# Kernel tuning notes

Hardware: AMD Instinct MI355X
Metric: run time of the kernel (lower is better)

The kernel has to match this reference:

```python
import jax, jax.numpy as jnp
import numpy as np

D_IN, HID = 128, 256
N_A, N_T = 120000, 30000
E_AT, E_TA, E_AA = 2_000_000, 2_000_000, 3_000_000
OUTS = [("artist", 129), ("style", 32), ("genre", 18)]


def setup_inputs() -> dict:
    key = jax.random.key(0)
    ks = jax.random.split(key, 32)

    def w(k, shape, fan_in):
        return jax.random.normal(k, shape, jnp.float32) / np.float32(np.sqrt(fan_in))

    def edges(k, e, n_src, n_dst):
        k1, k2 = jax.random.split(k)
        return jnp.stack([jax.random.randint(k1, (e,), 0, n_src),
                          jax.random.randint(k2, (e,), 0, n_dst)]).astype(jnp.int32)

    inp = {}
    inp["x_artwork"] = jax.random.normal(ks[0], (N_A, D_IN), jnp.float32)
    inp["x_tag"] = jax.random.normal(ks[1], (N_T, D_IN), jnp.float32)
    inp["edge_at"] = edges(ks[2], E_AT, N_A, N_T)
    inp["edge_ta"] = edges(ks[3], E_TA, N_T, N_A)
    inp["edge_aa"] = edges(ks[4], E_AA, N_A, N_A)
    # layer-1 weights shared shape across 3 gnns (G) and 3 relations (R): [G,R,din,H]
    inp["Wl1"] = w(ks[5], (3, 3, D_IN, HID), D_IN)
    inp["Wr1"] = w(ks[6], (3, 3, D_IN, HID), D_IN)
    inp["b1"] = jnp.zeros((3, 3, HID), jnp.float32)
    for i, (name, o) in enumerate(OUTS):
        inp[f"Wl2_{name}"] = w(ks[7 + 3 * i], (3, HID, o), HID)
        inp[f"Wr2_{name}"] = w(ks[8 + 3 * i], (3, HID, o), HID)
        inp[f"b2_{name}"] = jnp.zeros((3, o), jnp.float32)
    return inp


def _seg_mean(feat, dst, n):
    # PyG mean aggregation: sum over in-edges / count, 0 for isolated nodes
    s = jax.ops.segment_sum(feat, dst, num_segments=n)
    c = jax.ops.segment_sum(jnp.ones((dst.shape[0], 1), feat.dtype), dst, num_segments=n)
    return s / jnp.maximum(c, 1.0)


def _hetero_sage(xa, xt, e_at, e_ta, e_aa, Wl, Wr, b):
    # Wl/Wr: [3, din, dout] (rel order: at, ta, aa), b: [3, dout]
    m_at = _seg_mean(xa[e_at[0]], e_at[1], xt.shape[0])
    h_t = m_at @ Wl[0] + b[0] + xt @ Wr[0]
    m_ta = _seg_mean(xt[e_ta[0]], e_ta[1], xa.shape[0])
    m_aa = _seg_mean(xa[e_aa[0]], e_aa[1], xa.shape[0])
    h_a = (m_ta @ Wl[1] + b[1] + xa @ Wr[1]) + (m_aa @ Wl[2] + b[2] + xa @ Wr[2])
    return h_a, h_t


def _dropout(x, key, rate=0.5):
    keep = jax.random.bernoulli(key, 1.0 - rate, x.shape)
    return jnp.where(keep, x / (1.0 - rate), jnp.zeros((), x.dtype))


def _gnn(g, xa, xt, e_at, e_ta, e_aa, Wl1, Wr1, b1, Wl2, Wr2, b2):
    h_a, h_t = _hetero_sage(xa, xt, e_at, e_ta, e_aa, Wl1, Wr1, b1)
    h_a, h_t = jax.nn.relu(h_a), jax.nn.relu(h_t)
    k1, k2 = jax.random.split(jax.random.fold_in(jax.random.key(42), g))
    h_a, h_t = _dropout(h_a, k1), _dropout(h_t, k2)
    o_a, o_t = _hetero_sage(h_a, h_t, e_at, e_ta, e_aa, Wl2, Wr2, b2)
    return jax.nn.log_softmax(o_a, axis=1), jax.nn.log_softmax(o_t, axis=1)


def reference(x_artwork, x_tag, edge_at, edge_ta, edge_aa, Wl1, Wr1, b1,
              Wl2_artist, Wr2_artist, b2_artist,
              Wl2_style, Wr2_style, b2_style,
              Wl2_genre, Wr2_genre, b2_genre):
    l2 = [(Wl2_artist, Wr2_artist, b2_artist),
          (Wl2_style, Wr2_style, b2_style),
          (Wl2_genre, Wr2_genre, b2_genre)]
    outs = []
    for g in range(3):
        Wl2, Wr2, b2 = l2[g]
        o_a, o_t = _gnn(g, x_artwork, x_tag, edge_at, edge_ta, edge_aa,
                        Wl1[g], Wr1[g], b1[g], Wl2, Wr2, b2)
        outs.extend([o_a, o_t])
    return tuple(outs)
```

## Files before the change

### kernel.cpp

```cpp
#include <hip/hip_runtime.h>
#include <stdint.h>
#include <stddef.h>

typedef unsigned short bf16;
typedef __attribute__((ext_vector_type(8))) short short8;
typedef __attribute__((ext_vector_type(4))) float f32x4;

__device__ __forceinline__ float bf2f(unsigned short u){
  union { uint32_t i; float f; } x; x.i = ((uint32_t)u) << 16; return x.f;
}
__device__ __forceinline__ unsigned short f2bf(float f){
  union { float f; uint32_t i; } x; x.f = f;
  uint32_t r = x.i + 0x7FFFu + ((x.i >> 16) & 1u);
  return (unsigned short)(r >> 16);
}
__device__ __forceinline__ uint32_t pk2(float a, float b){
  return (uint32_t)f2bf(a) | ((uint32_t)f2bf(b) << 16);
}

__device__ __forceinline__ uint8_t f2fp8(float f){
  uint32_t b = __float_as_uint(f);
  uint32_t s = (b >> 24) & 0x80u;
  uint32_t x = b & 0x7fffffffu;
  if (x >= 0x43e00000u) return (uint8_t)(s | 0x7eu);
  if (x < 0x3c800000u){
    uint32_t q = (uint32_t)rintf(__uint_as_float(x) * 512.f);
    return (uint8_t)(s | q);
  }
  uint32_t lsb = (x >> 20) & 1u;
  x += 0x7ffffu + lsb;
  uint32_t u = (((x >> 23) - 120u) << 3) | ((x >> 20) & 7u);
  if (u > 0x7eu) u = 0x7eu;
  return (uint8_t)(s | u);
}
__device__ __forceinline__ float fp8d(uint8_t u){
  uint32_t e = (u >> 3) & 15u, m = u & 7u;
  float v = (e == 0) ? (float)m * 0.001953125f
                     : ldexpf((float)(8u + m), (int)e - 10);
  return (u & 0x80u) ? -v : v;
}

__host__ __device__ __forceinline__ uint32_t rotl32_(uint32_t x, int d){
  return (x << d) | (x >> (32 - d));
}
__host__ __device__ inline void tf2x32(uint32_t k0, uint32_t k1, uint32_t x0, uint32_t x1,
                                       uint32_t* o0, uint32_t* o1){
  uint32_t k2 = k0 ^ k1 ^ 0x1BD11BDAu;
#define TF_R4(ra,rb,rc,rd) \
  x0 += x1; x1 = rotl32_(x1,ra); x1 ^= x0; \
  x0 += x1; x1 = rotl32_(x1,rb); x1 ^= x0; \
  x0 += x1; x1 = rotl32_(x1,rc); x1 ^= x0; \
  x0 += x1; x1 = rotl32_(x1,rd); x1 ^= x0;
  x0 += k0; x1 += k1;
  TF_R4(13,15,26,6)  x0 += k1; x1 += k2 + 1u;
  TF_R4(17,29,16,24) x0 += k2; x1 += k0 + 2u;
  TF_R4(13,15,26,6)  x0 += k0; x1 += k1 + 3u;
  TF_R4(17,29,16,24) x0 += k1; x1 += k2 + 4u;
  TF_R4(13,15,26,6)  x0 += k2; x1 += k0 + 5u;
  *o0 = x0; *o1 = x1;
#undef TF_R4
}

__global__ void k_zeroi(int* __restrict__ p, int n){
  int i = blockIdx.x * 256 + threadIdx.x;
  if (i < n) p[i] = 0;
}
__global__ void k_f2bf(const float* __restrict__ in, bf16* __restrict__ out, int n4){
  int i = blockIdx.x * 256 + threadIdx.x;
  if (i < n4){
    float4 v = ((const float4*)in)[i];
    ushort4 u; u.x = f2bf(v.x); u.y = f2bf(v.y); u.z = f2bf(v.z); u.w = f2bf(v.w);
    ((ushort4*)out)[i] = u;
  }
}

__global__ void k_deg(const int* __restrict__ dst, int* __restrict__ deg, int E){
  int i = blockIdx.x * 256 + threadIdx.x;
  if (i < E) atomicAdd(&deg[dst[i]], 1);
}
__global__ __launch_bounds__(256)
void k_scan_partial(const int* __restrict__ in, int* __restrict__ exc,
                    int* __restrict__ bsum, int n){
  __shared__ int tmp[256];
  int t = threadIdx.x, i = blockIdx.x * 256 + t;
  int v = (i < n) ? in[i] : 0;
  tmp[t] = v; __syncthreads();
  #pragma unroll
  for (int off = 1; off < 256; off <<= 1){
    int u = (t >= off) ? tmp[t - off] : 0; __syncthreads();
    tmp[t] += u; __syncthreads();
  }
  if (i < n) exc[i] = tmp[t] - v;
  if (t == 255) bsum[blockIdx.x] = tmp[255];
}
__global__ __launch_bounds__(1024)
void k_scan_bsum(int* __restrict__ bsum, int nb, int* __restrict__ total_out){
  __shared__ int tmp[1024];
  int t = threadIdx.x;
  int v = (t < nb) ? bsum[t] : 0;
  tmp[t] = v; __syncthreads();
  #pragma unroll
  for (int off = 1; off < 1024; off <<= 1){
    int u = (t >= off) ? tmp[t - off] : 0; __syncthreads();
    tmp[t] += u; __syncthreads();
  }
  if (t < nb) bsum[t] = tmp[t] - v;
  if (t == 1023) *total_out = tmp[1023];
}
__global__ void k_scan_add(int* __restrict__ exc, const int* __restrict__ bsum, int n){
  int i = blockIdx.x * 256 + threadIdx.x;
  if (i < n) exc[i] += bsum[blockIdx.x];
}
__global__ void k_fill(const int* __restrict__ src, const int* __restrict__ dst,
                       const int* __restrict__ rs, int* __restrict__ cur,
                       int* __restrict__ cs, int E){
  int i = blockIdx.x * 256 + threadIdx.x;
  if (i < E){
    int d = dst[i];
    int p = atomicAdd(&cur[d], 1);
    cs[rs[d] + p] = src[i];
  }
}

__global__ __launch_bounds__(64)
void k_agg128b(const bf16* __restrict__ X, const int* __restrict__ rs,
               const int* __restrict__ cs, bf16* __restrict__ out){
  int node = blockIdx.x, lane = threadIdx.x;
  int s0 = rs[node], s1 = rs[node + 1];
  float ax = 0.f, ay = 0.f;
  int e = s0;
  for (; e + 4 <= s1; e += 4){
    int c0 = cs[e], c1 = cs[e+1], c2 = cs[e+2], c3 = cs[e+3];
    uint32_t v0 = ((const uint32_t*)(X + (size_t)c0 * 128))[lane];
    uint32_t v1 = ((const uint32_t*)(X + (size_t)c1 * 128))[lane];
    uint32_t v2 = ((const uint32_t*)(X + (size_t)c2 * 128))[lane];
    uint32_t v3 = ((const uint32_t*)(X + (size_t)c3 * 128))[lane];
    ax += bf2f((unsigned short)(v0 & 0xffffu)) + bf2f((unsigned short)(v1 & 0xffffu))
        + bf2f((unsigned short)(v2 & 0xffffu)) + bf2f((unsigned short)(v3 & 0xffffu));
    ay += bf2f((unsigned short)(v0 >> 16)) + bf2f((unsigned short)(v1 >> 16))
        + bf2f((unsigned short)(v2 >> 16)) + bf2f((unsigned short)(v3 >> 16));
  }
  for (; e < s1; ++e){
    uint32_t v = ((const uint32_t*)(X + (size_t)cs[e] * 128))[lane];
    ax += bf2f((unsigned short)(v & 0xffffu));
    ay += bf2f((unsigned short)(v >> 16));
  }
  float inv = 1.f / fmaxf((float)(s1 - s0), 1.f);
  ((uint32_t*)(out + (size_t)node * 128))[lane] = pk2(ax * inv, ay * inv);
}

__global__ void k_wt1a(const float* __restrict__ Wl1g, const float* __restrict__ Wr1g,
                       bf16* __restrict__ dst){
  int n = blockIdx.y, k = blockIdx.x * 128 + threadIdx.x;
  int seg = k >> 7, kk = k & 127;
  float v;
  if (seg == 0)      v = Wl1g[(size_t)(128 + kk) * 256 + n];
  else if (seg == 1) v = Wl1g[(size_t)(256 + kk) * 256 + n];
  else               v = Wr1g[(size_t)(128 + kk) * 256 + n] + Wr1g[(size_t)(256 + kk) * 256 + n];
  dst[(size_t)n * 384 + k] = f2bf(v);
}
__global__ void k_wt1t(const float* __restrict__ Wl1g, const float* __restrict__ Wr1g,
                       bf16* __restrict__ dst){
  int n = blockIdx.y, k = blockIdx.x * 128 + threadIdx.x;
  int kk = k & 127;
  float v = (k < 128) ? Wl1g[(size_t)kk * 256 + n] : Wr1g[(size_t)kk * 256 + n];
  dst[(size_t)n * 256 + k] = f2bf(v);
}
__global__ void k_wt2a(const float* __restrict__ Wl2g, const float* __restrict__ Wr2g,
                       int O, bf16* __restrict__ dst){
  int n = blockIdx.y, k = blockIdx.x * 128 + threadIdx.x;
  int strip = n / O, r = n - strip * O;
  float v;
  if (strip == 0)      v = Wl2g[(size_t)k * O + r];
  else if (strip == 1) v = Wl2g[(size_t)512 * O + (size_t)k * O + r];
  else                 v = Wr2g[(size_t)256 * O + (size_t)k * O + r]
                         + Wr2g[(size_t)512 * O + (size_t)k * O + r];
  dst[(size_t)n * 256 + k] = f2bf(v);
}
__global__ void k_wt2t(const float* __restrict__ Wl2g, const float* __restrict__ Wr2g,
                       int O, bf16* __restrict__ dst){
  int n = blockIdx.y, k = blockIdx.x * 128 + threadIdx.x;
  int strip = n / O, r = n - strip * O;
  float v = (strip == 0) ? Wl2g[(size_t)256 * O + (size_t)k * O + r]
                         : Wr2g[(size_t)k * O + r];
  dst[(size_t)n * 256 + k] = f2bf(v);
}
__global__ void k_bias(const float* __restrict__ b1g, const float* __restrict__ b2g,
                       int O, float* __restrict__ bc1, float* __restrict__ bc2){
  int t = threadIdx.x;
  bc1[t] = b1g[256 + t] + b1g[512 + t];
  if (t < O) bc2[t] = b2g[O + t] + b2g[2 * O + t];
}

template<int EPI>
__global__ __launch_bounds__(256)
void k_gemm_mfma(const bf16* __restrict__ A0, const bf16* __restrict__ A1,
                 const bf16* __restrict__ A2, int lda,
                 const bf16* __restrict__ Bt, int ldb,
                 int M, int N, int Ktot,
                 bf16* __restrict__ hC,
                 uint8_t* __restrict__ z0, uint8_t* __restrict__ z1,
                 float* __restrict__ outF, const float* __restrict__ bias,
                 int O, int zoff, uint32_t dk0, uint32_t dk1){
  __shared__ bf16 As[128][40];
  __shared__ bf16 Bs[64][40];
  const int tid = threadIdx.x;
  const int w = tid >> 6, l = tid & 63;
  const int r0 = blockIdx.y * 128, c0 = blockIdx.x * 64;

  f32x4 acc[2][4] = {};

  const int sm = tid >> 1, sk = (tid & 1) * 16;
  const int bn = tid >> 2, bk = (tid & 3) * 8;
  const int arow = r0 + sm, brow = c0 + bn;
  const int lr = l & 15, g8 = (l >> 4) * 8;

  for (int kk = 0; kk < Ktot; kk += 32){
    const int seg = kk >> 7, koff = (kk & 127) + sk;
    const bf16* Ap = (seg == 0) ? A0 : ((seg == 1) ? A1 : A2);
    uint4 wa0 = {0,0,0,0}, wa1 = {0,0,0,0};
    if (arow < M){
      const uint4* p = (const uint4*)(Ap + (size_t)arow * lda + koff);
      wa0 = p[0]; wa1 = p[1];
    }
    uint4 wb = {0,0,0,0};
    if (brow < N) wb = *(const uint4*)(Bt + (size_t)brow * ldb + kk + bk);
    __syncthreads();
    *(uint4*)&As[sm][sk]     = wa0;
    *(uint4*)&As[sm][sk + 8] = wa1;
    *(uint4*)&Bs[bn][bk]     = wb;
    __syncthreads();
    short8 a0 = *(const short8*)&As[w * 32      + lr][g8];
    short8 a1 = *(const short8*)&As[w * 32 + 16 + lr][g8];
    short8 b0 = *(const short8*)&Bs[     lr][g8];
    short8 b1 = *(const short8*)&Bs[16 + lr][g8];
    short8 b2 = *(const short8*)&Bs[32 + lr][g8];
    short8 b3 = *(const short8*)&Bs[48 + lr][g8];
    acc[0][0] = __builtin_amdgcn_mfma_f32_16x16x32_bf16(a0, b0, acc[0][0], 0, 0, 0);
    acc[0][1] = __builtin_amdgcn_mfma_f32_16x16x32_bf16(a0, b1, acc[0][1], 0, 0, 0);
    acc[0][2] = __builtin_amdgcn_mfma_f32_16x16x32_bf16(a0, b2, acc[0][2], 0, 0, 0);
    acc[0][3] = __builtin_amdgcn_mfma_f32_16x16x32_bf16(a0, b3, acc[0][3], 0, 0, 0);
    acc[1][0] = __builtin_amdgcn_mfma_f32_16x16x32_bf16(a1, b0, acc[1][0], 0, 0, 0);
    acc[1][1] = __builtin_amdgcn_mfma_f32_16x16x32_bf16(a1, b1, acc[1][1], 0, 0, 0);
    acc[1][2] = __builtin_amdgcn_mfma_f32_16x16x32_bf16(a1, b2, acc[1][2], 0, 0, 0);
    acc[1][3] = __builtin_amdgcn_mfma_f32_16x16x32_bf16(a1, b3, acc[1][3], 0, 0, 0);
  }
  #pragma unroll
  for (int rt = 0; rt < 2; ++rt){
    #pragma unroll
    for (int ct = 0; ct < 4; ++ct){
      #pragma unroll
      for (int r = 0; r < 4; ++r){
        int row = r0 + w * 32 + rt * 16 + (l >> 4) * 4 + r;
        int col = c0 + ct * 16 + lr;
        if (row < M && col < N){
          float v = acc[rt][ct][r];
          if (EPI == 0){
            v += bias[col];
            uint32_t o0, o1;
            tf2x32(dk0, dk1, 0u, (uint32_t)(row * 256 + col), &o0, &o1);
            float a = fmaxf(v, 0.f) * 2.f;
            hC[(size_t)row * 256 + col] = ((o0 ^ o1) >> 31) ? (bf16)0 : f2bf(a);
          } else {
            int s = (col >= O) + (EPI == 1 ? (col >= 2 * O) : 0);
            int lc = col - s * O;
            const int fs = (EPI == 1) ? 2 : 1;
            if (s == fs){
              outF[(size_t)row * O + lc] = v + bias[lc];
            } else {
              uint8_t* d = (s == 0) ? z0 : z1;
              d[(size_t)row * 192 + zoff + lc] = f2fp8(v);
            }
          }
        }
      }
    }
  }
}

__global__ __launch_bounds__(192)
void k_assemble_t(const uint8_t* __restrict__ z, const int* __restrict__ rs,
                  const int* __restrict__ cs,
                  float* __restrict__ o0, float* __restrict__ o1, float* __restrict__ o2){
  __shared__ float lut[256];
  __shared__ float sb[179];
  __shared__ float lse[3];
  const int node = blockIdx.x, t = threadIdx.x;
  lut[t] = fp8d((uint8_t)t);
  if (t < 64) lut[t + 192] = fp8d((uint8_t)(t + 192));
  const bool act = t < 179;
  const int h = (t < 129) ? 0 : ((t < 161) ? 1 : 2);
  const int base = (h == 0) ? 0 : ((h == 1) ? 129 : 161);
  const int Oh = (h == 0) ? 129 : ((h == 1) ? 32 : 18);
  const int s0 = rs[node], s1 = rs[node + 1];
  __syncthreads();
  float acc = 0.f;
  int e = s0;
  for (; e + 4 <= s1; e += 4){
    size_t c0 = (size_t)cs[e] * 192, c1 = (size_t)cs[e+1] * 192;
    size_t c2 = (size_t)cs[e+2] * 192, c3 = (size_t)cs[e+3] * 192;
    if (act){
      float v0 = lut[z[c0 + t]], v1 = lut[z[c1 + t]];
      float v2 = lut[z[c2 + t]], v3 = lut[z[c3 + t]];
      acc += (v0 + v1) + (v2 + v3);
    }
  }
  for (; e < s1; ++e)
    if (act) acc += lut[z[(size_t)cs[e] * 192 + t]];
  const float inv = 1.f / fmaxf((float)(s1 - s0), 1.f);
  float* orow = ((h == 0) ? o0 : ((h == 1) ? o1 : o2)) + (size_t)node * Oh + (t - base);
  float v = 0.f;
  if (act) v = *orow + acc * inv;
  if (act) sb[t] = v;
  __syncthreads();
  const int wv = t >> 6, ln = t & 63;
  {
    const int b = (wv == 0) ? 0 : ((wv == 1) ? 129 : 161);
    const int W = (wv == 0) ? 129 : ((wv == 1) ? 32 : 18);
    float m = -3.4e38f;
    for (int i = ln; i < W; i += 64) m = fmaxf(m, sb[b + i]);
    #pragma unroll
    for (int o = 32; o; o >>= 1) m = fmaxf(m, __shfl_xor(m, o));
    float s = 0.f;
    for (int i = ln; i < W; i += 64) s += expf(sb[b + i] - m);
    #pragma unroll
    for (int o = 32; o; o >>= 1) s += __shfl_xor(s, o);
    if (ln == 0) lse[wv] = m + logf(s);
  }
  __syncthreads();
  if (act) *orow = v - lse[h];
}

__global__ __launch_bounds__(192)
void k_assemble_a(const uint8_t* __restrict__ zT, const uint8_t* __restrict__ zA,
                  const int* __restrict__ rs_ta, const int* __restrict__ cs_ta,
                  const int* __restrict__ rs_aa, const int* __restrict__ cs_aa,
                  float* __restrict__ o0, float* __restrict__ o1, float* __restrict__ o2){
  __shared__ float lut[256];
  __shared__ float sb[179];
  __shared__ float lse[3];
  const int node = blockIdx.x, t = threadIdx.x;
  lut[t] = fp8d((uint8_t)t);
  if (t < 64) lut[t + 192] = fp8d((uint8_t)(t + 192));
  const bool act = t < 179;
  const int h = (t < 129) ? 0 : ((t < 161) ? 1 : 2);
  const int base = (h == 0) ? 0 : ((h == 1) ? 129 : 161);
  const int Oh = (h == 0) ? 129 : ((h == 1) ? 32 : 18);
  __syncthreads();
  float accT = 0.f, accA = 0.f;
  int s0 = rs_ta[node], s1 = rs_ta[node + 1];
  int e = s0;
  for (; e + 4 <= s1; e += 4){
    size_t c0 = (size_t)cs_ta[e] * 192, c1 = (size_t)cs_ta[e+1] * 192;
    size_t c2 = (size_t)cs_ta[e+2] * 192, c3 = (size_t)cs_ta[e+3] * 192;
    if (act){
      float v0 = lut[zT[c0 + t]], v1 = lut[zT[c1 + t]];
      float v2 = lut[zT[c2 + t]], v3 = lut[zT[c3 + t]];
      accT += (v0 + v1) + (v2 + v3);
    }
  }
  for (; e < s1; ++e)
    if (act) accT += lut[zT[(size_t)cs_ta[e] * 192 + t]];
  const float invT = 1.f / fmaxf((float)(s1 - s0), 1.f);
  s0 = rs_aa[node]; s1 = rs_aa[node + 1];
  e = s0;
  for (; e + 4 <= s1; e += 4){
    size_t c0 = (size_t)cs_aa[e] * 192, c1 = (size_t)cs_aa[e+1] * 192;
    size_t c2 = (size_t)cs_aa[e+2] * 192, c3 = (size_t)cs_aa[e+3] * 192;
    if (act){
      float v0 = lut[zA[c0 + t]], v1 = lut[zA[c1 + t]];
      float v2 = lut[zA[c2 + t]], v3 = lut[zA[c3 + t]];
      accA += (v0 + v1) + (v2 + v3);
    }
  }
  for (; e < s1; ++e)
    if (act) accA += lut[zA[(size_t)cs_aa[e] * 192 + t]];
  const float invA = 1.f / fmaxf((float)(s1 - s0), 1.f);
  float* orow = ((h == 0) ? o0 : ((h == 1) ? o1 : o2)) + (size_t)node * Oh + (t - base);
  float v = 0.f;
  if (act) v = *orow + accT * invT + accA * invA;
  if (act) sb[t] = v;
  __syncthreads();
  const int wv = t >> 6, ln = t & 63;
  {
    const int b = (wv == 0) ? 0 : ((wv == 1) ? 129 : 161);
    const int W = (wv == 0) ? 129 : ((wv == 1) ? 32 : 18);
    float m = -3.4e38f;
    for (int i = ln; i < W; i += 64) m = fmaxf(m, sb[b + i]);
    #pragma unroll
    for (int o = 32; o; o >>= 1) m = fmaxf(m, __shfl_xor(m, o));
    float s = 0.f;
    for (int i = ln; i < W; i += 64) s += expf(sb[b + i] - m);
    #pragma unroll
    for (int o = 32; o; o >>= 1) s += __shfl_xor(s, o);
    if (ln == 0) lse[wv] = m + logf(s);
  }
  __syncthreads();
  if (act) *orow = v - lse[h];
}

extern "C" void kernel_launch(void* const* d_in, const int* in_sizes, int n_in,
                              void* d_out, int out_size, void* d_ws, size_t ws_size,
                              hipStream_t stream){
  (void)n_in; (void)out_size; (void)ws_size;
  const float* xa  = (const float*)d_in[0];
  const float* xt  = (const float*)d_in[1];
  const int*   e_at = (const int*)d_in[2];
  const int*   e_ta = (const int*)d_in[3];
  const int*   e_aa = (const int*)d_in[4];
  const float* Wl1 = (const float*)d_in[5];
  const float* Wr1 = (const float*)d_in[6];
  const float* b1  = (const float*)d_in[7];
  const float* Wl2_[3] = {(const float*)d_in[8],  (const float*)d_in[11], (const float*)d_in[14]};
  const float* Wr2_[3] = {(const float*)d_in[9],  (const float*)d_in[12], (const float*)d_in[15]};
  const float* b2_[3]  = {(const float*)d_in[10], (const float*)d_in[13], (const float*)d_in[16]};

  const int NA = in_sizes[0] / 128;
  const int NT = in_sizes[1] / 128;
  const int EAT = in_sizes[2] / 2, ETA = in_sizes[3] / 2, EAA = in_sizes[4] / 2;
  const int Ov[3] = {129, 32, 18};
  const int og[3] = {0, 129, 161};

  char* Wp = (char*)d_ws;
  size_t off = 0;
  auto alloc = [&](size_t bytes)->char*{
    char* p = Wp + off; off = (off + bytes + 255) & ~(size_t)255; return p;
  };
  bf16* xa_b = (bf16*)alloc((size_t)NA * 128 * 2);
  bf16* xt_b = (bf16*)alloc((size_t)NT * 128 * 2);
  bf16* m_at = (bf16*)alloc((size_t)NT * 128 * 2);
  bf16* m_ta = (bf16*)alloc((size_t)NA * 128 * 2);
  bf16* m_aa = (bf16*)alloc((size_t)NA * 128 * 2);
  bf16* h_a  = (bf16*)alloc((size_t)NA * 256 * 2);
  bf16* h_t  = (bf16*)alloc((size_t)NT * 256 * 2);
  uint8_t* zA_at = (uint8_t*)alloc((size_t)NA * 192);
  uint8_t* zT_ta = (uint8_t*)alloc((size_t)NT * 192);
  uint8_t* zA_aa = (uint8_t*)alloc((size_t)NA * 192);
  bf16* Bt_ha = (bf16*)alloc((size_t)256 * 384 * 2);
  bf16* Bt_ht = (bf16*)alloc((size_t)256 * 256 * 2);
  bf16* BT2a  = (bf16*)alloc((size_t)3 * 129 * 256 * 2);
  bf16* BT2t  = (bf16*)alloc((size_t)2 * 129 * 256 * 2);
  float* bc1  = (float*)alloc(256 * 4);
  float* bc2  = (float*)alloc(129 * 4);
  int* rs_at  = (int*)alloc((size_t)(NT + 1) * 4);
  int* rs_ta  = (int*)alloc((size_t)(NA + 1) * 4);
  int* rs_aa  = (int*)alloc((size_t)(NA + 1) * 4);
  int* cur_at = (int*)alloc((size_t)NT * 4);
  int* cur_ta = (int*)alloc((size_t)NA * 4);
  int* cur_aa = (int*)alloc((size_t)NA * 4);
  int* bsum   = (int*)alloc(2048 * 4);
  int* cs_at  = (int*)alloc((size_t)EAT * 4);
  int* cs_ta  = (int*)alloc((size_t)ETA * 4);
  int* cs_aa  = (int*)alloc((size_t)EAA * 4);

  k_f2bf<<<(NA * 128 / 4 + 255) / 256, 256, 0, stream>>>(xa, xa_b, NA * 128 / 4);
  k_f2bf<<<(NT * 128 / 4 + 255) / 256, 256, 0, stream>>>(xt, xt_b, NT * 128 / 4);

  auto build_csr = [&](const int* edges, int E, int n, int* rs, int* cur, int* cs){
    int ebl = (E + 255) / 256, nbl = (n + 255) / 256;
    k_zeroi<<<nbl, 256, 0, stream>>>(cur, n);
    k_deg<<<ebl, 256, 0, stream>>>(edges + E, cur, E);
    k_scan_partial<<<nbl, 256, 0, stream>>>(cur, rs, bsum, n);
    k_scan_bsum<<<1, 1024, 0, stream>>>(bsum, nbl, rs + n);
    k_scan_add<<<nbl, 256, 0, stream>>>(rs, bsum, n);
    k_zeroi<<<nbl, 256, 0, stream>>>(cur, n);
    k_fill<<<ebl, 256, 0, stream>>>(edges, edges + E, rs, cur, cs, E);
  };
  build_csr(e_at, EAT, NT, rs_at, cur_at, cs_at);
  build_csr(e_ta, ETA, NA, rs_ta, cur_ta, cs_ta);
  build_csr(e_aa, EAA, NA, rs_aa, cur_aa, cs_aa);

  k_agg128b<<<NT, 64, 0, stream>>>(xa_b, rs_at, cs_at, m_at);
  k_agg128b<<<NA, 64, 0, stream>>>(xt_b, rs_ta, cs_ta, m_ta);
  k_agg128b<<<NA, 64, 0, stream>>>(xa_b, rs_aa, cs_aa, m_aa);

  size_t offA[3], offT[3], cum = 0;
  for (int g = 0; g < 3; ++g){
    offA[g] = cum; offT[g] = cum + (size_t)NA * Ov[g];
    cum += (size_t)(NA + NT) * Ov[g];
  }

  for (int g = 0; g < 3; ++g){
    const int O = Ov[g];
    float* outA = (float*)d_out + offA[g];
    float* outT = (float*)d_out + offT[g];
    const float* Wl1g = Wl1 + (size_t)(3 * g) * 128 * 256;
    const float* Wr1g = Wr1 + (size_t)(3 * g) * 128 * 256;
    const float* b1g  = b1  + (size_t)(3 * g) * 256;

    k_wt1a<<<dim3(3, 256), 128, 0, stream>>>(Wl1g, Wr1g, Bt_ha);
    k_wt1t<<<dim3(2, 256), 128, 0, stream>>>(Wl1g, Wr1g, Bt_ht);
    k_wt2a<<<dim3(2, 3 * O), 128, 0, stream>>>(Wl2_[g], Wr2_[g], O, BT2a);
    k_wt2t<<<dim3(2, 2 * O), 128, 0, stream>>>(Wl2_[g], Wr2_[g], O, BT2t);
    k_bias<<<1, 256, 0, stream>>>(b1g, b2_[g], O, bc1, bc2);

    uint32_t kg0, kg1, ka0, ka1, kt0, kt1;
    tf2x32(0u, 42u, 0u, (uint32_t)g, &kg0, &kg1);
    tf2x32(kg0, kg1, 0u, 0u, &ka0, &ka1);
    tf2x32(kg0, kg1, 0u, 1u, &kt0, &kt1);

    k_gemm_mfma<0><<<dim3(4, (NA + 127) / 128), 256, 0, stream>>>(
        m_ta, m_aa, xa_b, 128, Bt_ha, 384, NA, 256, 384,
        h_a, nullptr, nullptr, nullptr, bc1, 0, 0, ka0, ka1);
    k_gemm_mfma<0><<<dim3(4, (NT + 127) / 128), 256, 0, stream>>>(
        m_at, xt_b, xt_b, 128, Bt_ht, 256, NT, 256, 256,
        h_t, nullptr, nullptr, nullptr, b1g, 0, 0, kt0, kt1);

    k_gemm_mfma<1><<<dim3((3 * O + 63) / 64, (NA + 127) / 128), 256, 0, stream>>>(
        h_a, h_a + 128, h_a, 256, BT2a, 256, NA, 3 * O, 256,
        nullptr, zA_at, zA_aa, outA, bc2, O, og[g], 0, 0);
    k_gemm_mfma<2><<<dim3((2 * O + 63) / 64, (NT + 127) / 128), 256, 0, stream>>>(
        h_t, h_t + 128, h_t, 256, BT2t, 256, NT, 2 * O, 256,
        nullptr, zT_ta, nullptr, outT, b2_[g], O, og[g], 0, 0);
  }

  k_assemble_t<<<NT, 192, 0, stream>>>(zA_at, rs_at, cs_at,
                                       (float*)d_out + offT[0], (float*)d_out + offT[1],
                                       (float*)d_out + offT[2]);
  k_assemble_a<<<NA, 192, 0, stream>>>(zT_ta, zA_aa, rs_ta, cs_ta, rs_aa, cs_aa,
                                       (float*)d_out + offA[0], (float*)d_out + offA[1],
                                       (float*)d_out + offA[2]);
}
```

Baseline: 2.168 ms.

## Aggregate layer-1 neighbors from fp8 features, use hardware fp8 converts, widen GEMM tiles

```diff
diff --git a/kernel.cpp b/kernel.cpp
--- a/kernel.cpp
+++ b/kernel.cpp
@@ -18,7 +18,7 @@
   return (uint32_t)f2bf(a) | ((uint32_t)f2bf(b) << 16);
 }
 
-__device__ __forceinline__ uint8_t f2fp8(float f){
+__device__ __forceinline__ uint8_t f2fp8_sw(float f){
   uint32_t b = __float_as_uint(f);
   uint32_t s = (b >> 24) & 0x80u;
   uint32_t x = b & 0x7fffffffu;
@@ -33,11 +33,49 @@
   if (u > 0x7eu) u = 0x7eu;
   return (uint8_t)(s | u);
 }
+__device__ __forceinline__ float fp8_dec1_sw(uint32_t u){
+  uint32_t e = (u >> 3) & 15u, m = u & 7u;
+  float v = e ? __uint_as_float(((e + 120u) << 23) | (m << 20))
+              : (float)m * 0.001953125f;
+  return (u & 0x80u) ? -v : v;
+}
 __device__ __forceinline__ float fp8d(uint8_t u){
-  uint32_t e = (u >> 3) & 15u, m = u & 7u;
-  float v = (e == 0) ? (float)m * 0.001953125f
-                     : ldexpf((float)(8u + m), (int)e - 10);
-  return (u & 0x80u) ? -v : v;
+  return fp8_dec1_sw((uint32_t)u);
+}
+
+#if __has_builtin(__builtin_amdgcn_cvt_pk_f32_fp8) && __has_builtin(__builtin_amdgcn_cvt_pk_fp8_f32)
+#define FP8_HW 1
+#else
+#define FP8_HW 0
+#endif
+
+__device__ __forceinline__ void fp8_dec4(uint32_t w, float* o){
+#if FP8_HW
+  auto lo = __builtin_amdgcn_cvt_pk_f32_fp8((int)w, false);
+  auto hi = __builtin_amdgcn_cvt_pk_f32_fp8((int)w, true);
+  o[0] = lo[0]; o[1] = lo[1]; o[2] = hi[0]; o[3] = hi[1];
+#else
+  o[0] = fp8_dec1_sw(w & 0xffu);        o[1] = fp8_dec1_sw((w >> 8) & 0xffu);
+  o[2] = fp8_dec1_sw((w >> 16) & 0xffu); o[3] = fp8_dec1_sw(w >> 24);
+#endif
+}
+__device__ __forceinline__ uint8_t fp8_enc1(float v){
+#if FP8_HW
+  return (uint8_t)(__builtin_amdgcn_cvt_pk_fp8_f32(v, v, 0, false) & 0xff);
+#else
+  return f2fp8_sw(v);
+#endif
+}
+__device__ __forceinline__ uint32_t fp8_enc4(float a, float b, float c, float d){
+#if FP8_HW
+  int w = 0;
+  w = __builtin_amdgcn_cvt_pk_fp8_f32(a, b, w, false);
+  w = __builtin_amdgcn_cvt_pk_fp8_f32(c, d, w, true);
+  return (uint32_t)w;
+#else
+  return (uint32_t)f2fp8_sw(a) | ((uint32_t)f2fp8_sw(b) << 8)
+       | ((uint32_t)f2fp8_sw(c) << 16) | ((uint32_t)f2fp8_sw(d) << 24);
+#endif
 }
 
 __host__ __device__ __forceinline__ uint32_t rotl32_(uint32_t x, int d){
@@ -73,6 +111,13 @@
     ((ushort4*)out)[i] = u;
   }
 }
+__global__ void k_f2fp8(const float* __restrict__ in, uint8_t* __restrict__ out, int n4){
+  int i = blockIdx.x * 256 + threadIdx.x;
+  if (i < n4){
+    float4 v = ((const float4*)in)[i];
+    ((uint32_t*)out)[i] = fp8_enc4(v.x, v.y, v.z, v.w);
+  }
+}
 
 __global__ void k_deg(const int* __restrict__ dst, int* __restrict__ deg, int E){
   int i = blockIdx.x * 256 + threadIdx.x;
@@ -123,30 +168,38 @@
 }
 
 __global__ __launch_bounds__(64)
-void k_agg128b(const bf16* __restrict__ X, const int* __restrict__ rs,
-               const int* __restrict__ cs, bf16* __restrict__ out){
-  int node = blockIdx.x, lane = threadIdx.x;
-  int s0 = rs[node], s1 = rs[node + 1];
-  float ax = 0.f, ay = 0.f;
-  int e = s0;
-  for (; e + 4 <= s1; e += 4){
-    int c0 = cs[e], c1 = cs[e+1], c2 = cs[e+2], c3 = cs[e+3];
-    uint32_t v0 = ((const uint32_t*)(X + (size_t)c0 * 128))[lane];
-    uint32_t v1 = ((const uint32_t*)(X + (size_t)c1 * 128))[lane];
-    uint32_t v2 = ((const uint32_t*)(X + (size_t)c2 * 128))[lane];
-    uint32_t v3 = ((const uint32_t*)(X + (size_t)c3 * 128))[lane];
-    ax += bf2f((unsigned short)(v0 & 0xffffu)) + bf2f((unsigned short)(v1 & 0xffffu))
-        + bf2f((unsigned short)(v2 & 0xffffu)) + bf2f((unsigned short)(v3 & 0xffffu));
-    ay += bf2f((unsigned short)(v0 >> 16)) + bf2f((unsigned short)(v1 >> 16))
-        + bf2f((unsigned short)(v2 >> 16)) + bf2f((unsigned short)(v3 >> 16));
-  }
-  for (; e < s1; ++e){
-    uint32_t v = ((const uint32_t*)(X + (size_t)cs[e] * 128))[lane];
-    ax += bf2f((unsigned short)(v & 0xffffu));
-    ay += bf2f((unsigned short)(v >> 16));
-  }
-  float inv = 1.f / fmaxf((float)(s1 - s0), 1.f);
-  ((uint32_t*)(out + (size_t)node * 128))[lane] = pk2(ax * inv, ay * inv);
+void k_agg128_8(const uint8_t* __restrict__ X8, const int* __restrict__ rs,
+                const int* __restrict__ cs, bf16* __restrict__ out){
+  const int node = blockIdx.x, lane = threadIdx.x;
+  const int hl = lane >> 5, cl = lane & 31;
+  const int s0 = rs[node], s1 = rs[node + 1];
+  const int last = s1 - 1;
+  float a[4] = {0.f, 0.f, 0.f, 0.f};
+  for (int e = s0; e < s1; e += 8){
+    uint32_t w[4];
+    #pragma unroll
+    for (int j = 0; j < 4; ++j){
+      int i = e + j * 2 + hl;
+      int idx = (i < s1) ? i : last;
+      uint32_t ww = *(const uint32_t*)(X8 + (size_t)cs[idx] * 128 + (cl << 2));
+      w[j] = (i < s1) ? ww : 0u;
+    }
+    #pragma unroll
+    for (int j = 0; j < 4; ++j){
+      float d[4];
+      fp8_dec4(w[j], d);
+      a[0] += d[0]; a[1] += d[1]; a[2] += d[2]; a[3] += d[3];
+    }
+  }
+  #pragma unroll
+  for (int j = 0; j < 4; ++j) a[j] += __shfl_xor(a[j], 32);
+  if (lane < 32){
+    float inv = 1.f / fmaxf((float)(s1 - s0), 1.f);
+    ushort4 u;
+    u.x = f2bf(a[0] * inv); u.y = f2bf(a[1] * inv);
+    u.z = f2bf(a[2] * inv); u.w = f2bf(a[3] * inv);
+    *(ushort4*)(out + (size_t)node * 128 + (cl << 2)) = u;
+  }
 }
 
 __global__ void k_wt1a(const float* __restrict__ Wl1g, const float* __restrict__ Wr1g,
@@ -203,16 +256,16 @@
                  float* __restrict__ outF, const float* __restrict__ bias,
                  int O, int zoff, uint32_t dk0, uint32_t dk1){
   __shared__ bf16 As[128][40];
-  __shared__ bf16 Bs[64][40];
+  __shared__ bf16 Bs[128][40];
   const int tid = threadIdx.x;
   const int w = tid >> 6, l = tid & 63;
-  const int r0 = blockIdx.y * 128, c0 = blockIdx.x * 64;
-
-  f32x4 acc[2][4] = {};
+  const int wr = w >> 1, wc = w & 1;
+  const int r0 = blockIdx.y * 128, c0 = blockIdx.x * 128;
+
+  f32x4 acc[4][4] = {};
 
   const int sm = tid >> 1, sk = (tid & 1) * 16;
-  const int bn = tid >> 2, bk = (tid & 3) * 8;
-  const int arow = r0 + sm, brow = c0 + bn;
+  const int arow = r0 + sm, brow = c0 + sm;
   const int lr = l & 15, g8 = (l >> 4) * 8;
 
   for (int kk = 0; kk < Ktot; kk += 32){
@@ -223,36 +276,37 @@
       const uint4* p = (const uint4*)(Ap + (size_t)arow * lda + koff);
       wa0 = p[0]; wa1 = p[1];
     }
-    uint4 wb = {0,0,0,0};
-    if (brow < N) wb = *(const uint4*)(Bt + (size_t)brow * ldb + kk + bk);
+    uint4 wb0 = {0,0,0,0}, wb1 = {0,0,0,0};
+    if (brow < N){
+      const uint4* p = (const uint4*)(Bt + (size_t)brow * ldb + kk + sk);
+      wb0 = p[0]; wb1 = p[1];
+    }
     __syncthreads();
     *(uint4*)&As[sm][sk]     = wa0;
     *(uint4*)&As[sm][sk + 8] = wa1;
-    *(uint4*)&Bs[bn][bk]     = wb;
+    *(uint4*)&Bs[sm][sk]     = wb0;
+    *(uint4*)&Bs[sm][sk + 8] = wb1;
     __syncthreads();
-    short8 a0 = *(const short8*)&As[w * 32      + lr][g8];
-    short8 a1 = *(const short8*)&As[w * 32 + 16 + lr][g8];
-    short8 b0 = *(const short8*)&Bs[     lr][g8];
-    short8 b1 = *(const short8*)&Bs[16 + lr][g8];
-    short8 b2 = *(const short8*)&Bs[32 + lr][g8];
-    short8 b3 = *(const short8*)&Bs[48 + lr][g8];
-    acc[0][0] = __builtin_amdgcn_mfma_f32_16x16x32_bf16(a0, b0, acc[0][0], 0, 0, 0);
-    acc[0][1] = __builtin_amdgcn_mfma_f32_16x16x32_bf16(a0, b1, acc[0][1], 0, 0, 0);
-    acc[0][2] = __builtin_amdgcn_mfma_f32_16x16x32_bf16(a0, b2, acc[0][2], 0, 0, 0);
-    acc[0][3] = __builtin_amdgcn_mfma_f32_16x16x32_bf16(a0, b3, acc[0][3], 0, 0, 0);
-    acc[1][0] = __builtin_amdgcn_mfma_f32_16x16x32_bf16(a1, b0, acc[1][0], 0, 0, 0);
-    acc[1][1] = __builtin_amdgcn_mfma_f32_16x16x32_bf16(a1, b1, acc[1][1], 0, 0, 0);
-    acc[1][2] = __builtin_amdgcn_mfma_f32_16x16x32_bf16(a1, b2, acc[1][2], 0, 0, 0);
-    acc[1][3] = __builtin_amdgcn_mfma_f32_16x16x32_bf16(a1, b3, acc[1][3], 0, 0, 0);
+    short8 af[4], bf[4];
+    #pragma unroll
+    for (int f = 0; f < 4; ++f){
+      af[f] = *(const short8*)&As[wr * 64 + f * 16 + lr][g8];
+      bf[f] = *(const short8*)&Bs[wc * 64 + f * 16 + lr][g8];
+    }
+    #pragma unroll
+    for (int i = 0; i < 4; ++i)
+      #pragma unroll
+      for (int j = 0; j < 4; ++j)
+        acc[i][j] = __builtin_amdgcn_mfma_f32_16x16x32_bf16(af[i], bf[j], acc[i][j], 0, 0, 0);
   }
   #pragma unroll
-  for (int rt = 0; rt < 2; ++rt){
+  for (int rt = 0; rt < 4; ++rt){
     #pragma unroll
     for (int ct = 0; ct < 4; ++ct){
       #pragma unroll
       for (int r = 0; r < 4; ++r){
-        int row = r0 + w * 32 + rt * 16 + (l >> 4) * 4 + r;
-        int col = c0 + ct * 16 + lr;
+        int row = r0 + wr * 64 + rt * 16 + (l >> 4) * 4 + r;
+        int col = c0 + wc * 64 + ct * 16 + lr;
         if (row < M && col < N){
           float v = acc[rt][ct][r];
           if (EPI == 0){
@@ -269,7 +323,7 @@
               outF[(size_t)row * O + lc] = v + bias[lc];
             } else {
               uint8_t* d = (s == 0) ? z0 : z1;
-              d[(size_t)row * 192 + zoff + lc] = f2fp8(v);
+              d[(size_t)row * 192 + zoff + lc] = fp8_enc1(v);
             }
           }
         }
@@ -426,7 +480,10 @@
   auto alloc = [&](size_t bytes)->char*{
     char* p = Wp + off; off = (off + bytes + 255) & ~(size_t)255; return p;
   };
-  bf16* xa_b = (bf16*)alloc((size_t)NA * 128 * 2);
+  char* slot0 = alloc((size_t)NA * 128 * 2);
+  uint8_t* xa_8 = (uint8_t*)slot0;
+  uint8_t* xt_8 = (uint8_t*)(slot0 + (size_t)NA * 128);
+  bf16* xa_b = (bf16*)slot0;
   bf16* xt_b = (bf16*)alloc((size_t)NT * 128 * 2);
   bf16* m_at = (bf16*)alloc((size_t)NT * 128 * 2);
   bf16* m_ta = (bf16*)alloc((size_t)NA * 128 * 2);
@@ -453,8 +510,8 @@
   int* cs_ta  = (int*)alloc((size_t)ETA * 4);
   int* cs_aa  = (int*)alloc((size_t)EAA * 4);
 
-  k_f2bf<<<(NA * 128 / 4 + 255) / 256, 256, 0, stream>>>(xa, xa_b, NA * 128 / 4);
-  k_f2bf<<<(NT * 128 / 4 + 255) / 256, 256, 0, stream>>>(xt, xt_b, NT * 128 / 4);
+  k_f2fp8<<<(NA * 128 / 4 + 255) / 256, 256, 0, stream>>>(xa, xa_8, NA * 128 / 4);
+  k_f2fp8<<<(NT * 128 / 4 + 255) / 256, 256, 0, stream>>>(xt, xt_8, NT * 128 / 4);
 
   auto build_csr = [&](const int* edges, int E, int n, int* rs, int* cur, int* cs){
     int ebl = (E + 255) / 256, nbl = (n + 255) / 256;
@@ -470,9 +527,12 @@
   build_csr(e_ta, ETA, NA, rs_ta, cur_ta, cs_ta);
   build_csr(e_aa, EAA, NA, rs_aa, cur_aa, cs_aa);
 
-  k_agg128b<<<NT, 64, 0, stream>>>(xa_b, rs_at, cs_at, m_at);
-  k_agg128b<<<NA, 64, 0, stream>>>(xt_b, rs_ta, cs_ta, m_ta);
-  k_agg128b<<<NA, 64, 0, stream>>>(xa_b, rs_aa, cs_aa, m_aa);
+  k_agg128_8<<<NT, 64, 0, stream>>>(xa_8, rs_at, cs_at, m_at);
+  k_agg128_8<<<NA, 64, 0, stream>>>(xt_8, rs_ta, cs_ta, m_ta);
+  k_agg128_8<<<NA, 64, 0, stream>>>(xa_8, rs_aa, cs_aa, m_aa);
+
+  k_f2bf<<<(NA * 128 / 4 + 255) / 256, 256, 0, stream>>>(xa, xa_b, NA * 128 / 4);
+  k_f2bf<<<(NT * 128 / 4 + 255) / 256, 256, 0, stream>>>(xt, xt_b, NT * 128 / 4);
 
   size_t offA[3], offT[3], cum = 0;
   for (int g = 0; g < 3; ++g){
@@ -499,17 +559,17 @@
     tf2x32(kg0, kg1, 0u, 0u, &ka0, &ka1);
     tf2x32(kg0, kg1, 0u, 1u, &kt0, &kt1);
 
-    k_gemm_mfma<0><<<dim3(4, (NA + 127) / 128), 256, 0, stream>>>(
+    k_gemm_mfma<0><<<dim3(2, (NA + 127) / 128), 256, 0, stream>>>(
         m_ta, m_aa, xa_b, 128, Bt_ha, 384, NA, 256, 384,
         h_a, nullptr, nullptr, nullptr, bc1, 0, 0, ka0, ka1);
-    k_gemm_mfma<0><<<dim3(4, (NT + 127) / 128), 256, 0, stream>>>(
+    k_gemm_mfma<0><<<dim3(2, (NT + 127) / 128), 256, 0, stream>>>(
         m_at, xt_b, xt_b, 128, Bt_ht, 256, NT, 256, 256,
         h_t, nullptr, nullptr, nullptr, b1g, 0, 0, kt0, kt1);
 
-    k_gemm_mfma<1><<<dim3((3 * O + 63) / 64, (NA + 127) / 128), 256, 0, stream>>>(
+    k_gemm_mfma<1><<<dim3((3 * O + 127) / 128, (NA + 127) / 128), 256, 0, stream>>>(
         h_a, h_a + 128, h_a, 256, BT2a, 256, NA, 3 * O, 256,
         nullptr, zA_at, zA_aa, outA, bc2, O, og[g], 0, 0);
-    k_gemm_mfma<2><<<dim3((2 * O + 63) / 64, (NT + 127) / 128), 256, 0, stream>>>(
+    k_gemm_mfma<2><<<dim3((2 * O + 127) / 128, (NT + 127) / 128), 256, 0, stream>>>(
         h_t, h_t + 128, h_t, 256, BT2t, 256, NT, 2 * O, 256,
         nullptr, zT_ta, nullptr, outT, b2_[g], O, og[g], 0, 0);
   }
```

New measurement: 2.156 ms. Within noise of the previous version (-0.5%).
